# Performance work log

Measured on AMD Instinct MI355X. Metric: run time of the kernel, lower is better.

Reference implementation:

```python
import jax, jax.numpy as jnp
import numpy as np

NUM_HEADS = 8
ATTN_DIM = 512
DIM_HEAD = ATTN_DIM // NUM_HEADS
SCALE = DIM_HEAD ** -0.5
GN_EPS = 1e-5


def setup_inputs() -> dict:
    key = jax.random.key(0)
    k1, k2, k3 = jax.random.split(key, 3)
    B, H, W, C_IN, C_OUT = 8, 32, 32, 256, 256
    x = jax.random.normal(k1, (B, H, W, C_IN), dtype=jnp.float32)
    w_qkv = jax.random.normal(k2, (C_IN, 3 * ATTN_DIM), dtype=jnp.float32) * (C_IN ** -0.5)
    w_out = jax.random.normal(k3, (ATTN_DIM, C_OUT), dtype=jnp.float32) * (ATTN_DIM ** -0.5)
    b_out = jnp.zeros((C_OUT,), dtype=jnp.float32)
    gamma = jnp.ones((C_OUT,), dtype=jnp.float32)
    beta = jnp.zeros((C_OUT,), dtype=jnp.float32)
    return {"x": x, "w_qkv": w_qkv, "w_out": w_out, "b_out": b_out, "gamma": gamma, "beta": beta}


def reference(x, w_qkv, w_out, b_out, gamma, beta):
    B, H, W, _ = x.shape
    N = H * W
    # 1x1 conv QKV projection (no bias)
    qkv = jnp.einsum('bhwc,cd->bhwd', x, w_qkv)
    q, k, v = jnp.split(qkv, 3, axis=-1)
    # NHWC -> (B, heads, dim_head, HW), matching tf transpose+reshape
    def to_heads(t):
        return t.transpose(0, 3, 1, 2).reshape(B, NUM_HEADS, DIM_HEAD, N)
    q = to_heads(q) * SCALE
    k = to_heads(k)
    v = to_heads(v)
    # sim = q^T k over dim_head: (B, heads, N_q, N_k)
    sim = jnp.einsum('bhcn,bhcm->bhnm', q, k)
    attn = jax.nn.softmax(sim, axis=-1)  # includes the max-subtraction of the original
    # out = attn @ v^T: (B, heads, N, dim_head)
    out = jnp.einsum('bhnm,bhcm->bhnc', attn, v)
    # faithful tf.reshape((B,-1,H,W)) then NCHW->NHWC transpose
    out = out.reshape(B, -1, H, W).transpose(0, 2, 3, 1)  # (B, H, W, attn_dim)
    # output 1x1 conv (with bias) + GroupNorm(groups=1): normalize over (H, W, C) per sample
    y = jnp.einsum('bhwc,cd->bhwd', out, w_out) + b_out
    mean = jnp.mean(y, axis=(1, 2, 3), keepdims=True)
    var = jnp.var(y, axis=(1, 2, 3), keepdims=True)
    y = (y - mean) * jax.lax.rsqrt(var + GN_EPS)
    return y * gamma + beta
```

## Files before the change

kernel.cpp:

```cpp
#include <hip/hip_runtime.h>
#include <math.h>

#define NPOS   1024
#define CIN    256
#define DQKV   1536
#define ATTND  512
#define HEADS  8
#define DH     64
#define COUT   256
#define NBATCH 8
#define SCALE  0.125f
#define GN_EPS 1e-5f

typedef __attribute__((ext_vector_type(8))) __bf16 bf16x8;
typedef __attribute__((ext_vector_type(4))) __bf16 bf16x4;
typedef __attribute__((ext_vector_type(4))) float floatx4;
typedef __attribute__((ext_vector_type(8))) unsigned short ushort8;

#define OFF_WT   (4ull*1048576)
#define OFF_WOT  (4ull*1048576 + 786432ull)
#define OFF_QB   (5ull*1048576)
#define OFF_KB   (13ull*1048576)
#define OFF_VT   (29ull*1048576)
#define OFF_O2TT (45ull*1048576)
#define OFF_ST   (53ull*1048576)

__device__ inline ushort8 cvt_bf8(float4 a, float4 b) {
    bf16x8 o;
    o[0] = (__bf16)a.x; o[1] = (__bf16)a.y; o[2] = (__bf16)a.z; o[3] = (__bf16)a.w;
    o[4] = (__bf16)b.x; o[5] = (__bf16)b.y; o[6] = (__bf16)b.z; o[7] = (__bf16)b.w;
    return *(ushort8*)&o;
}

__global__ __launch_bounds__(256) void prep(
    const float* __restrict__ w_qkv, const float* __restrict__ w_out,
    unsigned short* __restrict__ wT, unsigned short* __restrict__ woT,
    float* __restrict__ stats)
{
    const int bid = blockIdx.x;
    const int t = threadIdx.x;
    __shared__ unsigned short tile[64][68];

    if (bid == 0) stats[t] = 0.0f;

    if (bid < 96) {
        const int n0 = (bid >> 2) * 64, k0 = (bid & 3) * 64;
        #pragma unroll
        for (int p = 0; p < 4; ++p) {
            const int row = p * 16 + (t >> 4);
            const int c = (t & 15) * 4;
            float4 a = *(const float4*)&w_qkv[(size_t)(k0 + row) * DQKV + n0 + c];
            float sv[4] = {a.x, a.y, a.z, a.w};
            #pragma unroll
            for (int j = 0; j < 4; ++j) {
                const float sc = (n0 + c + j) < 512 ? SCALE : 1.0f;
                __bf16 hb = (__bf16)(sv[j] * sc);
                tile[row][c + j] = *(unsigned short*)&hb;
            }
        }
        __syncthreads();
        const int nn = t >> 2;
        const int kc = (t & 3) * 16;
        unsigned short tmp[16];
        #pragma unroll
        for (int j = 0; j < 16; ++j) tmp[j] = tile[kc + j][nn];
        *(ushort8*)&wT[(size_t)(n0 + nn) * 256 + k0 + kc]     = *(ushort8*)&tmp[0];
        *(ushort8*)&wT[(size_t)(n0 + nn) * 256 + k0 + kc + 8] = *(ushort8*)&tmp[8];
        return;
    }

    const int idx = bid - 96;
    const int d0 = (idx & 3) * 64, k0 = (idx >> 2) * 64;
    #pragma unroll
    for (int p = 0; p < 4; ++p) {
        const int row = p * 16 + (t >> 4);
        const int c = (t & 15) * 4;
        float4 a = *(const float4*)&w_out[(size_t)(k0 + row) * COUT + d0 + c];
        float sv[4] = {a.x, a.y, a.z, a.w};
        #pragma unroll
        for (int j = 0; j < 4; ++j) {
            __bf16 hb = (__bf16)sv[j];
            tile[row][c + j] = *(unsigned short*)&hb;
        }
    }
    __syncthreads();
    {
        const int nn = t >> 2;
        const int kc = (t & 3) * 16;
        unsigned short tmp[16];
        #pragma unroll
        for (int j = 0; j < 16; ++j) tmp[j] = tile[kc + j][nn];
        *(ushort8*)&woT[(size_t)(d0 + nn) * 512 + k0 + kc]     = *(ushort8*)&tmp[0];
        *(ushort8*)&woT[(size_t)(d0 + nn) * 512 + k0 + kc + 8] = *(ushort8*)&tmp[8];
    }
}

__global__ __launch_bounds__(256) void qkv_gemm_mfma(
    const float* __restrict__ x, const __bf16* __restrict__ wT,
    __bf16* __restrict__ qb, __bf16* __restrict__ kb, __bf16* __restrict__ vT)
{
    const int t = threadIdx.x;
    const int w = t >> 6, lane = t & 63;
    const int col = lane & 15, qd = lane >> 4;
    const int wm = w >> 1, wn = w & 1;
    const int m0 = blockIdx.x * 128, n0 = blockIdx.y * 128;

    __shared__ __align__(16) unsigned short As[128][40];
    __shared__ __align__(16) unsigned short Bs[128][40];

    floatx4 zero4 = {0.f, 0.f, 0.f, 0.f};
    floatx4 acc[4][4];
    #pragma unroll
    for (int i = 0; i < 4; ++i)
        #pragma unroll
        for (int j = 0; j < 4; ++j) acc[i][j] = zero4;

    const int lrow = t >> 2, lc8 = (t & 3) * 8;

    float4 a0, a1, a2, a3;
    ushort8 breg[2];
    a0 = *(const float4*)&x[(size_t)(m0 + lrow) * 256 + lc8];
    a1 = *(const float4*)&x[(size_t)(m0 + lrow) * 256 + lc8 + 4];
    a2 = *(const float4*)&x[(size_t)(m0 + lrow + 64) * 256 + lc8];
    a3 = *(const float4*)&x[(size_t)(m0 + lrow + 64) * 256 + lc8 + 4];
    breg[0] = *(const ushort8*)&wT[(size_t)(n0 + lrow) * 256 + lc8];
    breg[1] = *(const ushort8*)&wT[(size_t)(n0 + lrow + 64) * 256 + lc8];

    for (int kk = 0; kk < 8; ++kk) {
        __syncthreads();
        *(ushort8*)&As[lrow][lc8]      = cvt_bf8(a0, a1);
        *(ushort8*)&As[lrow + 64][lc8] = cvt_bf8(a2, a3);
        *(ushort8*)&Bs[lrow][lc8]      = breg[0];
        *(ushort8*)&Bs[lrow + 64][lc8] = breg[1];
        __syncthreads();
        const int kn = (kk < 7) ? (kk + 1) * 32 : 0;
        a0 = *(const float4*)&x[(size_t)(m0 + lrow) * 256 + kn + lc8];
        a1 = *(const float4*)&x[(size_t)(m0 + lrow) * 256 + kn + lc8 + 4];
        a2 = *(const float4*)&x[(size_t)(m0 + lrow + 64) * 256 + kn + lc8];
        a3 = *(const float4*)&x[(size_t)(m0 + lrow + 64) * 256 + kn + lc8 + 4];
        breg[0] = *(const ushort8*)&wT[(size_t)(n0 + lrow) * 256 + kn + lc8];
        breg[1] = *(const ushort8*)&wT[(size_t)(n0 + lrow + 64) * 256 + kn + lc8];

        bf16x8 wf[4];
        #pragma unroll
        for (int ct = 0; ct < 4; ++ct)
            wf[ct] = *(const bf16x8*)&Bs[wn * 64 + ct * 16 + col][qd * 8];
        #pragma unroll
        for (int st = 0; st < 4; ++st) {
            bf16x8 xf = *(const bf16x8*)&As[wm * 64 + st * 16 + col][qd * 8];
            #pragma unroll
            for (int ct = 0; ct < 4; ++ct)
                acc[ct][st] = __builtin_amdgcn_mfma_f32_16x16x32_bf16(wf[ct], xf, acc[ct][st], 0, 0, 0);
        }
    }

    #pragma unroll
    for (int ct = 0; ct < 4; ++ct) {
        const int cbase = n0 + wn * 64 + ct * 16;
        const int sect = cbase >> 9;
        const int hh = (cbase >> 6) & 7;
        const int dd = (cbase & 63) + qd * 4;
        if (sect < 2) {
            __bf16* base = (sect == 0) ? qb : kb;
            #pragma unroll
            for (int st = 0; st < 4; ++st) {
                const int m = m0 + wm * 64 + st * 16 + col;
                const int b_ = m >> 10, n = m & 1023;
                bf16x4 o;
                #pragma unroll
                for (int r = 0; r < 4; ++r) o[r] = (__bf16)acc[ct][st][r];
                *(bf16x4*)&base[(((size_t)b_ * HEADS + hh) * NPOS + n) * DH + dd] = o;
            }
        } else {
            #pragma unroll
            for (int st = 0; st < 4; ++st) {
                const int m = m0 + wm * 64 + st * 16 + col;
                const int b_ = m >> 10, n = m & 1023;
                const size_t rowbase = ((size_t)(b_ * HEADS + hh) * DH + dd) * NPOS + n;
                #pragma unroll
                for (int r = 0; r < 4; ++r)
                    vT[rowbase + (size_t)r * NPOS] = (__bf16)acc[ct][st][r];
            }
        }
    }
}

__global__ __launch_bounds__(256, 2) void attn_mfma(
    const __bf16* __restrict__ qg, const __bf16* __restrict__ kg,
    const __bf16* __restrict__ vTg, __bf16* __restrict__ o2tT)
{
    const int bid = blockIdx.x;
    const int qblk = bid & 7, h = (bid >> 3) & 7, b = bid >> 6;
    const int bh = b * HEADS + h;
    const int t = threadIdx.x;
    const int w = t >> 6, lane = t & 63;
    const int col = lane & 15;
    const int qd = lane >> 4;

    __shared__ __align__(16) unsigned short Ks[64][72];
    __shared__ __align__(16) unsigned short Vts[64][72];
    __shared__ __align__(16) unsigned short ps[4][32][68];

    bf16x8 qf0[2], qf1[2];
    #pragma unroll
    for (int s = 0; s < 2; ++s) {
        const __bf16* qptr = qg + ((size_t)bh * NPOS + qblk * 128 + s * 64 + w * 16 + col) * DH;
        qf0[s] = *(const bf16x8*)(qptr + qd * 8);
        qf1[s] = *(const bf16x8*)(qptr + 32 + qd * 8);
    }

    const unsigned short* kbase  = (const unsigned short*)kg  + (size_t)bh * NPOS * DH;
    const unsigned short* vtbase = (const unsigned short*)vTg + (size_t)bh * DH * NPOS;

    const int r0 = t >> 3, c8 = (t & 7) * 8;

    ushort8 kreg[2], vreg[2];
    kreg[0] = *(const ushort8*)&kbase[(size_t)r0 * DH + c8];
    kreg[1] = *(const ushort8*)&kbase[(size_t)(r0 + 32) * DH + c8];
    vreg[0] = *(const ushort8*)&vtbase[(size_t)r0 * NPOS + c8];
    vreg[1] = *(const ushort8*)&vtbase[(size_t)(r0 + 32) * NPOS + c8];

    floatx4 zero4 = {0.f, 0.f, 0.f, 0.f};
    floatx4 accO[2][4];
    #pragma unroll
    for (int s = 0; s < 2; ++s)
        #pragma unroll
        for (int i = 0; i < 4; ++i) accO[s][i] = zero4;
    float lsum_acc[2] = {0.0f, 0.0f};

    for (int kt = 0; kt < 16; ++kt) {
        __syncthreads();
        *(ushort8*)&Ks[r0][c8]       = kreg[0];
        *(ushort8*)&Ks[r0 + 32][c8]  = kreg[1];
        *(ushort8*)&Vts[r0][c8]      = vreg[0];
        *(ushort8*)&Vts[r0 + 32][c8] = vreg[1];
        __syncthreads();

        const int ktn = (kt < 15) ? kt + 1 : 15;
        kreg[0] = *(const ushort8*)&kbase[(size_t)(ktn * 64 + r0) * DH + c8];
        kreg[1] = *(const ushort8*)&kbase[(size_t)(ktn * 64 + r0 + 32) * DH + c8];
        vreg[0] = *(const ushort8*)&vtbase[(size_t)r0 * NPOS + ktn * 64 + c8];
        vreg[1] = *(const ushort8*)&vtbase[(size_t)(r0 + 32) * NPOS + ktn * 64 + c8];

        floatx4 accS[2][4];
        #pragma unroll
        for (int mt = 0; mt < 4; ++mt) {
            bf16x8 kf0 = *(const bf16x8*)&Ks[mt * 16 + col][qd * 8];
            bf16x8 kf1 = *(const bf16x8*)&Ks[mt * 16 + col][32 + qd * 8];
            #pragma unroll
            for (int s = 0; s < 2; ++s) {
                accS[s][mt] = __builtin_amdgcn_mfma_f32_16x16x32_bf16(kf0, qf0[s], zero4, 0, 0, 0);
                accS[s][mt] = __builtin_amdgcn_mfma_f32_16x16x32_bf16(kf1, qf1[s], accS[s][mt], 0, 0, 0);
            }
        }

        #pragma unroll
        for (int s = 0; s < 2; ++s)
            #pragma unroll
            for (int mt = 0; mt < 4; ++mt) {
                bf16x4 pv;
                #pragma unroll
                for (int r = 0; r < 4; ++r) {
                    const float e = __expf(accS[s][mt][r]);
                    lsum_acc[s] += e;
                    pv[r] = (__bf16)e;
                }
                *(bf16x4*)&ps[w][s * 16 + col][mt * 16 + qd * 4] = pv;
            }

        bf16x8 pf0[2], pf1[2];
        #pragma unroll
        for (int s = 0; s < 2; ++s) {
            pf0[s] = *(const bf16x8*)&ps[w][s * 16 + col][qd * 8];
            pf1[s] = *(const bf16x8*)&ps[w][s * 16 + col][32 + qd * 8];
        }

        #pragma unroll
        for (int ct = 0; ct < 4; ++ct) {
            bf16x8 vf0 = *(const bf16x8*)&Vts[ct * 16 + col][qd * 8];
            bf16x8 vf1 = *(const bf16x8*)&Vts[ct * 16 + col][32 + qd * 8];
            #pragma unroll
            for (int s = 0; s < 2; ++s) {
                accO[s][ct] = __builtin_amdgcn_mfma_f32_16x16x32_bf16(vf0, pf0[s], accO[s][ct], 0, 0, 0);
                accO[s][ct] = __builtin_amdgcn_mfma_f32_16x16x32_bf16(vf1, pf1[s], accO[s][ct], 0, 0, 0);
            }
        }
    }

    float inv_l[2];
    #pragma unroll
    for (int s = 0; s < 2; ++s) {
        float l = lsum_acc[s];
        l += __shfl_xor(l, 16);
        l += __shfl_xor(l, 32);
        inv_l[s] = 1.0f / l;
    }

    unsigned short (*obuf)[8][68] = (unsigned short (*)[8][68])ps;
    __syncthreads();
    #pragma unroll
    for (int s = 0; s < 2; ++s)
        #pragma unroll
        for (int ct = 0; ct < 4; ++ct) {
            bf16x4 o;
            #pragma unroll
            for (int r = 0; r < 4; ++r) o[r] = (__bf16)(accO[s][ct][r] * inv_l[s]);
            *(bf16x4*)&obuf[col][s * 4 + w][ct * 16 + qd * 4] = o;
        }
    __syncthreads();
    const int chbase = h * 64 + qblk * 8;
    #pragma unroll
    for (int i = 0; i < 4; ++i) {
        const int p = i * 256 + t;
        const int pc = p >> 6, cc = p & 63;
        bf16x8 o;
        #pragma unroll
        for (int j = 0; j < 8; ++j) {
            unsigned short u = obuf[pc][j][cc];
            o[j] = *(__bf16*)&u;
        }
        *(bf16x8*)&o2tT[((size_t)b * NPOS + p) * ATTND + chbase] = o;
    }
}

__global__ __launch_bounds__(256) void out_mfma(
    const __bf16* __restrict__ a, const __bf16* __restrict__ woT,
    const float* __restrict__ b_out, float* __restrict__ y,
    float* __restrict__ stats)
{
    const int t = threadIdx.x;
    const int w = t >> 6, lane = t & 63;
    const int col = lane & 15, qd = lane >> 4;
    const int wm = w >> 1, wn = w & 1;
    const int m0 = blockIdx.x * 64, d0 = blockIdx.y * 64;
    const int b = blockIdx.x >> 4;

    __shared__ __align__(16) unsigned short As[64][72];
    __shared__ __align__(16) unsigned short Bs[64][72];
    __shared__ float reds[4], redq[4];

    floatx4 zero4 = {0.f, 0.f, 0.f, 0.f};
    floatx4 acc[2][2];
    #pragma unroll
    for (int i = 0; i < 2; ++i)
        #pragma unroll
        for (int j = 0; j < 2; ++j) acc[i][j] = zero4;

    const int lrow = t >> 2, lc = (t & 3) * 16;

    for (int k0 = 0; k0 < ATTND; k0 += 64) {
        __syncthreads();
        *(ushort8*)&As[lrow][lc]     = *(const ushort8*)&a[(size_t)(m0 + lrow) * ATTND + k0 + lc];
        *(ushort8*)&As[lrow][lc + 8] = *(const ushort8*)&a[(size_t)(m0 + lrow) * ATTND + k0 + lc + 8];
        *(ushort8*)&Bs[lrow][lc]     = *(const ushort8*)&woT[(size_t)(d0 + lrow) * ATTND + k0 + lc];
        *(ushort8*)&Bs[lrow][lc + 8] = *(const ushort8*)&woT[(size_t)(d0 + lrow) * ATTND + k0 + lc + 8];
        __syncthreads();
        bf16x8 af0[2], af1[2];
        #pragma unroll
        for (int mt = 0; mt < 2; ++mt) {
            af0[mt] = *(const bf16x8*)&As[wm * 32 + mt * 16 + col][qd * 8];
            af1[mt] = *(const bf16x8*)&As[wm * 32 + mt * 16 + col][32 + qd * 8];
        }
        #pragma unroll
        for (int nt = 0; nt < 2; ++nt) {
            bf16x8 bf0 = *(const bf16x8*)&Bs[wn * 32 + nt * 16 + col][qd * 8];
            bf16x8 bf1 = *(const bf16x8*)&Bs[wn * 32 + nt * 16 + col][32 + qd * 8];
            #pragma unroll
            for (int mt = 0; mt < 2; ++mt) {
                acc[mt][nt] = __builtin_amdgcn_mfma_f32_16x16x32_bf16(af0[mt], bf0, acc[mt][nt], 0, 0, 0);
                acc[mt][nt] = __builtin_amdgcn_mfma_f32_16x16x32_bf16(af1[mt], bf1, acc[mt][nt], 0, 0, 0);
            }
        }
    }

    float bias_n[2];
    #pragma unroll
    for (int nt = 0; nt < 2; ++nt) bias_n[nt] = b_out[d0 + wn * 32 + nt * 16 + col];

    float bsum = 0.0f, bsq = 0.0f;
    #pragma unroll
    for (int mt = 0; mt < 2; ++mt) {
        #pragma unroll
        for (int r = 0; r < 4; ++r) {
            const int m = m0 + wm * 32 + mt * 16 + qd * 4 + r;
            const int p = m & 1023;
            #pragma unroll
            for (int nt = 0; nt < 2; ++nt) {
                const int d = d0 + wn * 32 + nt * 16 + col;
                const float v = acc[mt][nt][r] + bias_n[nt];
                y[((size_t)b * NPOS + p) * COUT + d] = v;
                bsum += v;
                bsq  += v * v;
            }
        }
    }
    #pragma unroll
    for (int off = 1; off < 64; off <<= 1) {
        bsum += __shfl_xor(bsum, off);
        bsq  += __shfl_xor(bsq, off);
    }
    if (lane == 0) { reds[w] = bsum; redq[w] = bsq; }
    __syncthreads();
    if (t == 0) {
        atomicAdd(&stats[b * 16],       reds[0] + reds[1] + reds[2] + reds[3]);
        atomicAdd(&stats[128 + b * 16], redq[0] + redq[1] + redq[2] + redq[3]);
    }
}

__global__ __launch_bounds__(256) void gn_finalize(
    float* __restrict__ y, const float* __restrict__ stats,
    const float* __restrict__ gamma, const float* __restrict__ beta)
{
    const int idx = blockIdx.x * 256 + threadIdx.x;
    const int e = idx * 4;
    const int b_ = e >> 18;
    const int d = e & (COUT - 1);
    const float invn = 1.0f / (float)(NPOS * COUT);
    const float mean = stats[b_ * 16] * invn;
    const float var  = stats[128 + b_ * 16] * invn - mean * mean;
    const float rsig = rsqrtf(var + GN_EPS);
    float4 vv = *(float4*)&y[e];
    const float4 g  = *(const float4*)&gamma[d];
    const float4 bt = *(const float4*)&beta[d];
    vv.x = (vv.x - mean) * rsig * g.x + bt.x;
    vv.y = (vv.y - mean) * rsig * g.y + bt.y;
    vv.z = (vv.z - mean) * rsig * g.z + bt.z;
    vv.w = (vv.w - mean) * rsig * g.w + bt.w;
    *(float4*)&y[e] = vv;
}

extern "C" void kernel_launch(void* const* d_in, const int* in_sizes, int n_in,
                              void* d_out, int out_size, void* d_ws, size_t ws_size,
                              hipStream_t stream)
{
    const float* x     = (const float*)d_in[0];
    const float* w_qkv = (const float*)d_in[1];
    const float* w_out = (const float*)d_in[2];
    const float* b_out = (const float*)d_in[3];
    const float* gamma = (const float*)d_in[4];
    const float* beta  = (const float*)d_in[5];
    float* out = (float*)d_out;
    char* ws = (char*)d_ws;

    unsigned short* wT  = (unsigned short*)(ws + OFF_WT);
    unsigned short* woT = (unsigned short*)(ws + OFF_WOT);
    __bf16* qb  = (__bf16*)(ws + OFF_QB);
    __bf16* kb  = (__bf16*)(ws + OFF_KB);
    __bf16* vT  = (__bf16*)(ws + OFF_VT);
    __bf16* o2tT = (__bf16*)(ws + OFF_O2TT);
    float* stats = (float*)(ws + OFF_ST);

    prep         <<<dim3(128),    256, 0, stream>>>(w_qkv, w_out, wT, woT, stats);
    qkv_gemm_mfma<<<dim3(64, 12), 256, 0, stream>>>(x, (const __bf16*)wT, qb, kb, vT);
    attn_mfma    <<<dim3(512),    256, 0, stream>>>(qb, kb, vT, o2tT);
    out_mfma     <<<dim3(128, 4), 256, 0, stream>>>(o2tT, (const __bf16*)woT, b_out, out, stats);
    gn_finalize  <<<dim3(2048),   256, 0, stream>>>(out, stats, gamma, beta);
}
```

Baseline: 128.8 us.

## Double-buffer K/V via direct global-to-LDS loads with swizzle, exp2 softmax, MFMA row sums

Replaces the register-staged K/V tile loads in the attention kernel with global_load_lds direct-to-LDS copies into double-buffered, XOR-swizzled shared tiles, so the next tile loads while the current one is computed and one barrier per iteration is dropped. Folds log2(e) into the Q scale so the softmax can use a native exp2. Computes the row sums with an extra MFMA against a ones vector instead of scalar adds and shuffles, which sums the bf16-rounded probabilities. Also remaps block IDs so that blocks sharing a batch and head are spread apart in launch order. Risks include the extra LDS per block reducing occupancy and the row-sum change shifting numerics slightly.

```diff
diff --git a/kernel.cpp b/kernel.cpp
--- a/kernel.cpp
+++ b/kernel.cpp
@@ -17,6 +17,16 @@
 typedef __attribute__((ext_vector_type(4))) float floatx4;
 typedef __attribute__((ext_vector_type(8))) unsigned short ushort8;
 
+#if __has_builtin(__builtin_amdgcn_exp2f)
+#define EXP2(x) __builtin_amdgcn_exp2f(x)
+#else
+#define EXP2(x) exp2f(x)
+#endif
+
+#define GLOAD16(G, L) __builtin_amdgcn_global_load_lds( \
+    (const __attribute__((address_space(1))) void*)(G), \
+    (__attribute__((address_space(3))) void*)(L), 16, 0, 0)
+
 #define OFF_WT   (4ull*1048576)
 #define OFF_WOT  (4ull*1048576 + 786432ull)
 #define OFF_QB   (5ull*1048576)
@@ -53,7 +63,7 @@
             float sv[4] = {a.x, a.y, a.z, a.w};
             #pragma unroll
             for (int j = 0; j < 4; ++j) {
-                const float sc = (n0 + c + j) < 512 ? SCALE : 1.0f;
+                const float sc = (n0 + c + j) < 512 ? (SCALE * 1.44269504088896f) : 1.0f;
                 __bf16 hb = (__bf16)(sv[j] * sc);
                 tile[row][c + j] = *(unsigned short*)&hb;
             }
@@ -190,15 +200,16 @@
     const __bf16* __restrict__ vTg, __bf16* __restrict__ o2tT)
 {
     const int bid = blockIdx.x;
-    const int qblk = bid & 7, h = (bid >> 3) & 7, b = bid >> 6;
+    const int rid = (bid & 7) * 64 + (bid >> 3);
+    const int qblk = rid & 7, h = (rid >> 3) & 7, b = rid >> 6;
     const int bh = b * HEADS + h;
     const int t = threadIdx.x;
     const int w = t >> 6, lane = t & 63;
     const int col = lane & 15;
     const int qd = lane >> 4;
 
-    __shared__ __align__(16) unsigned short Ks[64][72];
-    __shared__ __align__(16) unsigned short Vts[64][72];
+    __shared__ __align__(16) unsigned short Kbuf[2][64][64];
+    __shared__ __align__(16) unsigned short Vbuf[2][64][64];
     __shared__ __align__(16) unsigned short ps[4][32][68];
 
     bf16x8 qf0[2], qf1[2];
@@ -209,16 +220,21 @@
         qf1[s] = *(const bf16x8*)(qptr + 32 + qd * 8);
     }
 
-    const unsigned short* kbase  = (const unsigned short*)kg  + (size_t)bh * NPOS * DH;
-    const unsigned short* vtbase = (const unsigned short*)vTg + (size_t)bh * DH * NPOS;
-
-    const int r0 = t >> 3, c8 = (t & 7) * 8;
-
-    ushort8 kreg[2], vreg[2];
-    kreg[0] = *(const ushort8*)&kbase[(size_t)r0 * DH + c8];
-    kreg[1] = *(const ushort8*)&kbase[(size_t)(r0 + 32) * DH + c8];
-    vreg[0] = *(const ushort8*)&vtbase[(size_t)r0 * NPOS + c8];
-    vreg[1] = *(const ushort8*)&vtbase[(size_t)(r0 + 32) * NPOS + c8];
+    const char* kByte = (const char*)kg  + (size_t)bh * NPOS * DH * 2;
+    const char* vByte = (const char*)vTg + (size_t)bh * DH * NPOS * 2;
+    const int rsub = lane >> 3;
+    const int csw  = ((lane & 7) * 16) ^ (rsub << 4);
+    const char* ksrc0 = kByte + (size_t)(w * 8 + rsub) * 128  + csw;
+    const char* vsrc0 = vByte + (size_t)(w * 8 + rsub) * 2048 + csw;
+
+#define STAGE(B, KT) do {                                                    \
+    const char* ks_ = ksrc0 + (size_t)(KT) * 8192;                           \
+    const char* vs_ = vsrc0 + (size_t)(KT) * 128;                            \
+    GLOAD16(ks_,         &Kbuf[B][0][0] + w * 512);                          \
+    GLOAD16(ks_ + 4096,  &Kbuf[B][0][0] + 2048 + w * 512);                   \
+    GLOAD16(vs_,         &Vbuf[B][0][0] + w * 512);                          \
+    GLOAD16(vs_ + 65536, &Vbuf[B][0][0] + 2048 + w * 512);                   \
+} while (0)
 
     floatx4 zero4 = {0.f, 0.f, 0.f, 0.f};
     floatx4 accO[2][4];
@@ -226,27 +242,28 @@
     for (int s = 0; s < 2; ++s)
         #pragma unroll
         for (int i = 0; i < 4; ++i) accO[s][i] = zero4;
-    float lsum_acc[2] = {0.0f, 0.0f};
-
+    floatx4 accL[2] = {zero4, zero4};
+    bf16x8 ones8;
+    #pragma unroll
+    for (int j = 0; j < 8; ++j) ones8[j] = (__bf16)1.0f;
+
+    const int swzc = (col & 7) << 4;
+    const int offF0 = (qd * 16) ^ swzc;
+    const int offF1 = (64 + qd * 16) ^ swzc;
+
+    STAGE(0, 0);
+    __syncthreads();
+
+    int cur = 0;
     for (int kt = 0; kt < 16; ++kt) {
-        __syncthreads();
-        *(ushort8*)&Ks[r0][c8]       = kreg[0];
-        *(ushort8*)&Ks[r0 + 32][c8]  = kreg[1];
-        *(ushort8*)&Vts[r0][c8]      = vreg[0];
-        *(ushort8*)&Vts[r0 + 32][c8] = vreg[1];
-        __syncthreads();
-
-        const int ktn = (kt < 15) ? kt + 1 : 15;
-        kreg[0] = *(const ushort8*)&kbase[(size_t)(ktn * 64 + r0) * DH + c8];
-        kreg[1] = *(const ushort8*)&kbase[(size_t)(ktn * 64 + r0 + 32) * DH + c8];
-        vreg[0] = *(const ushort8*)&vtbase[(size_t)r0 * NPOS + ktn * 64 + c8];
-        vreg[1] = *(const ushort8*)&vtbase[(size_t)(r0 + 32) * NPOS + ktn * 64 + c8];
+        if (kt < 15) STAGE(cur ^ 1, kt + 1);
 
         floatx4 accS[2][4];
         #pragma unroll
         for (int mt = 0; mt < 4; ++mt) {
-            bf16x8 kf0 = *(const bf16x8*)&Ks[mt * 16 + col][qd * 8];
-            bf16x8 kf1 = *(const bf16x8*)&Ks[mt * 16 + col][32 + qd * 8];
+            const char* krow = (const char*)&Kbuf[cur][mt * 16 + col][0];
+            bf16x8 kf0 = *(const bf16x8*)(krow + offF0);
+            bf16x8 kf1 = *(const bf16x8*)(krow + offF1);
             #pragma unroll
             for (int s = 0; s < 2; ++s) {
                 accS[s][mt] = __builtin_amdgcn_mfma_f32_16x16x32_bf16(kf0, qf0[s], zero4, 0, 0, 0);
@@ -260,11 +277,7 @@
             for (int mt = 0; mt < 4; ++mt) {
                 bf16x4 pv;
                 #pragma unroll
-                for (int r = 0; r < 4; ++r) {
-                    const float e = __expf(accS[s][mt][r]);
-                    lsum_acc[s] += e;
-                    pv[r] = (__bf16)e;
-                }
+                for (int r = 0; r < 4; ++r) pv[r] = (__bf16)EXP2(accS[s][mt][r]);
                 *(bf16x4*)&ps[w][s * 16 + col][mt * 16 + qd * 4] = pv;
             }
 
@@ -273,28 +286,29 @@
         for (int s = 0; s < 2; ++s) {
             pf0[s] = *(const bf16x8*)&ps[w][s * 16 + col][qd * 8];
             pf1[s] = *(const bf16x8*)&ps[w][s * 16 + col][32 + qd * 8];
+            accL[s] = __builtin_amdgcn_mfma_f32_16x16x32_bf16(ones8, pf0[s], accL[s], 0, 0, 0);
+            accL[s] = __builtin_amdgcn_mfma_f32_16x16x32_bf16(ones8, pf1[s], accL[s], 0, 0, 0);
         }
 
         #pragma unroll
         for (int ct = 0; ct < 4; ++ct) {
-            bf16x8 vf0 = *(const bf16x8*)&Vts[ct * 16 + col][qd * 8];
-            bf16x8 vf1 = *(const bf16x8*)&Vts[ct * 16 + col][32 + qd * 8];
+            const char* vrow = (const char*)&Vbuf[cur][ct * 16 + col][0];
+            bf16x8 vf0 = *(const bf16x8*)(vrow + offF0);
+            bf16x8 vf1 = *(const bf16x8*)(vrow + offF1);
             #pragma unroll
             for (int s = 0; s < 2; ++s) {
                 accO[s][ct] = __builtin_amdgcn_mfma_f32_16x16x32_bf16(vf0, pf0[s], accO[s][ct], 0, 0, 0);
                 accO[s][ct] = __builtin_amdgcn_mfma_f32_16x16x32_bf16(vf1, pf1[s], accO[s][ct], 0, 0, 0);
             }
         }
-    }
+        __syncthreads();
+        cur ^= 1;
+    }
+#undef STAGE
 
     float inv_l[2];
     #pragma unroll
-    for (int s = 0; s < 2; ++s) {
-        float l = lsum_acc[s];
-        l += __shfl_xor(l, 16);
-        l += __shfl_xor(l, 32);
-        inv_l[s] = 1.0f / l;
-    }
+    for (int s = 0; s < 2; ++s) inv_l[s] = 1.0f / accL[s][0];
 
     unsigned short (*obuf)[8][68] = (unsigned short (*)[8][68])ps;
     __syncthreads();
```

After: 124.3 us. -3.6%, faster.
